# Optimization experiments

Measured on AMD Instinct MI355X. Metric: run time of the kernel, lower is better.

## Reference

```python
import jax, jax.numpy as jnp
import numpy as np

N_NODES = 50000
N_EDGES = 800000
D_IN = 64
D_OUT = 64


def setup_inputs() -> dict:
    key = jax.random.key(0)
    k = jax.random.split(key, 5)
    stdv = 1.0 / np.sqrt(D_OUT)
    X = jax.random.normal(k[0], (N_NODES, D_IN), jnp.float32)
    weights = jax.random.uniform(k[1], (D_IN, D_OUT), jnp.float32, -stdv, stdv)
    attention_w = jax.random.normal(k[2], (1, 1), jnp.float32)
    # edge list: row = destination (segment) ids, sorted (CSR-like); col = source ids
    row = jnp.sort(jax.random.randint(k[3], (N_EDGES,), 0, N_NODES, jnp.int32))
    col = jax.random.randint(k[4], (N_EDGES,), 0, N_NODES, jnp.int32)
    return {"X": X, "weights": weights, "attention_w": attention_w, "row": row, "col": col}


def reference(X, weights, attention_w, row, col):
    # dense linear
    Xp = X @ weights  # [N, D_OUT]
    # SDDMM: per-edge dot product between dst and src transformed features
    edge_feature = jnp.einsum('ed,ed->e', Xp[row], Xp[col])  # [E]
    # scale by scalar attention weight (n_heads = 1)
    edge_attn = edge_feature * attention_w[0, 0]  # [E]
    # SpMM aggregation: out[i] = sum_{e: row[e]=i} edge_attn[e] * Xp[col[e]]
    out = jax.ops.segment_sum(edge_attn[:, None] * Xp[col], row,
                              num_segments=X.shape[0])  # [N, D_OUT]
    return out
```

## Files before the change

### kernel.cpp

```cpp
#include <hip/hip_runtime.h>
#include <hip/hip_fp16.h>

#define D 64

typedef _Float16 h16;
typedef h16 h16x2 __attribute__((ext_vector_type(2)));

__device__ __forceinline__ h16x2 u2h(unsigned int u) {
    union { unsigned int i; h16x2 h; } t; t.i = u; return t.h;
}

__device__ __forceinline__ float dot8_f16(uint4 a, uint4 b, float c) {
#if __has_builtin(__builtin_amdgcn_fdot2)
    c = __builtin_amdgcn_fdot2(u2h(a.x), u2h(b.x), c, false);
    c = __builtin_amdgcn_fdot2(u2h(a.y), u2h(b.y), c, false);
    c = __builtin_amdgcn_fdot2(u2h(a.z), u2h(b.z), c, false);
    c = __builtin_amdgcn_fdot2(u2h(a.w), u2h(b.w), c, false);
    return c;
#else
    float2 t;
    t = __half22float2(*(const __half2*)&a.x); float2 s = __half22float2(*(const __half2*)&b.x);
    c = fmaf(t.x, s.x, c); c = fmaf(t.y, s.y, c);
    t = __half22float2(*(const __half2*)&a.y); s = __half22float2(*(const __half2*)&b.y);
    c = fmaf(t.x, s.x, c); c = fmaf(t.y, s.y, c);
    t = __half22float2(*(const __half2*)&a.z); s = __half22float2(*(const __half2*)&b.z);
    c = fmaf(t.x, s.x, c); c = fmaf(t.y, s.y, c);
    t = __half22float2(*(const __half2*)&a.w); s = __half22float2(*(const __half2*)&b.w);
    c = fmaf(t.x, s.x, c); c = fmaf(t.y, s.y, c);
    return c;
#endif
}

__device__ __forceinline__ void h8_to_f32(uint4 u, float f[8]) {
    float2 t;
    t = __half22float2(*(const __half2*)&u.x); f[0] = t.x; f[1] = t.y;
    t = __half22float2(*(const __half2*)&u.y); f[2] = t.x; f[3] = t.y;
    t = __half22float2(*(const __half2*)&u.z); f[4] = t.x; f[5] = t.y;
    t = __half22float2(*(const __half2*)&u.w); f[6] = t.x; f[7] = t.y;
}

__global__ __launch_bounds__(256) void prep_kernel(const float* __restrict__ X,
                                                   const float* __restrict__ W,
                                                   const int* __restrict__ row,
                                                   __half* __restrict__ Xp,
                                                   int* __restrict__ rowptr,
                                                   int nNodes, int nEdges,
                                                   int gemmBlocks) {
    if ((int)blockIdx.x >= gemmBlocks) {
        int e = (blockIdx.x - gemmBlocks) * 256 + threadIdx.x;
        if (e >= nEdges) return;
        int r = row[e];
        int rprev = (e == 0) ? -1 : row[e - 1];
        for (int q = rprev + 1; q <= r; ++q) rowptr[q] = e;
        if (e == nEdges - 1) {
            for (int q = r + 1; q <= nNodes; ++q) rowptr[q] = nEdges;
        }
        return;
    }
    int lane = threadIdx.x & 63;
    int wave = (blockIdx.x * 256 + threadIdx.x) >> 6;
    int nWaves = gemmBlocks * 4;

    float w[D];
#pragma unroll
    for (int k = 0; k < D; ++k) w[k] = W[k * D + lane];

    for (int r = wave; r < nNodes; r += nWaves) {
        int rr = __builtin_amdgcn_readfirstlane(r);
        const float4* xr = (const float4*)(X + (size_t)rr * D);
        float acc = 0.f;
#pragma unroll
        for (int k4 = 0; k4 < D / 4; ++k4) {
            float4 xv = xr[k4];
            acc = fmaf(xv.x, w[4 * k4 + 0], acc);
            acc = fmaf(xv.y, w[4 * k4 + 1], acc);
            acc = fmaf(xv.z, w[4 * k4 + 2], acc);
            acc = fmaf(xv.w, w[4 * k4 + 3], acc);
        }
        Xp[(size_t)rr * D + lane] = __float2half(acc);
    }
}

__global__ __launch_bounds__(256) void fused_kernel(const __half* __restrict__ Xp,
                                                    const int* __restrict__ rowptr,
                                                    const int* __restrict__ col,
                                                    const float* __restrict__ attn_w,
                                                    float* __restrict__ out,
                                                    int nNodes) {
    int lane = threadIdx.x & 63;
    int waveId = (blockIdx.x * 256 + threadIdx.x) >> 6;
    int g = lane >> 3;
    int j = lane & 7;

    int node = waveId * 8 + g;
    bool active = node < nNodes;
    int nd = active ? node : 0;

    int eStart = rowptr[nd];
    int eEnd   = active ? rowptr[nd + 1] : eStart;

    const uint4* XpV = (const uint4*)Xp;
    uint4 xr = XpV[(size_t)nd * 8 + j];

    float acc[8] = {0.f, 0.f, 0.f, 0.f, 0.f, 0.f, 0.f, 0.f};

    bool v[4]; uint4 raw[4];
#pragma unroll
    for (int u = 0; u < 4; ++u) {
        int ee = eStart + u;
        v[u] = ee < eEnd;
        int cc = col[v[u] ? ee : 0];
        raw[u] = XpV[(size_t)cc * 8 + j];
    }

    for (int e = eStart; e < eEnd; e += 4) {
        bool v2[4]; uint4 raw2[4];
#pragma unroll
        for (int u = 0; u < 4; ++u) {
            int ee = e + 4 + u;
            v2[u] = ee < eEnd;
            int cc = col[v2[u] ? ee : 0];
            raw2[u] = XpV[(size_t)cc * 8 + j];
        }
        float p[4];
#pragma unroll
        for (int u = 0; u < 4; ++u) p[u] = dot8_f16(xr, raw[u], 0.f);
#pragma unroll
        for (int off = 1; off < 8; off <<= 1)
#pragma unroll
            for (int u = 0; u < 4; ++u) p[u] += __shfl_xor(p[u], off, 64);
#pragma unroll
        for (int u = 0; u < 4; ++u) {
            float s = v[u] ? p[u] : 0.f;
            float xf[8]; h8_to_f32(raw[u], xf);
#pragma unroll
            for (int q = 0; q < 8; ++q) acc[q] = fmaf(s, xf[q], acc[q]);
        }
#pragma unroll
        for (int u = 0; u < 4; ++u) { v[u] = v2[u]; raw[u] = raw2[u]; }
    }

    if (active) {
        float attn = attn_w[0];
        float4* o = (float4*)(out + (size_t)node * D + 8 * j);
        o[0] = make_float4(attn * acc[0], attn * acc[1], attn * acc[2], attn * acc[3]);
        o[1] = make_float4(attn * acc[4], attn * acc[5], attn * acc[6], attn * acc[7]);
    }
}

extern "C" void kernel_launch(void* const* d_in, const int* in_sizes, int n_in,
                              void* d_out, int out_size, void* d_ws, size_t ws_size,
                              hipStream_t stream) {
    const float* X    = (const float*)d_in[0];
    const float* W    = (const float*)d_in[1];
    const float* attn = (const float*)d_in[2];
    const int*   row  = (const int*)d_in[3];
    const int*   col  = (const int*)d_in[4];
    float* out = (float*)d_out;

    int nNodes = in_sizes[0] / D;
    int nEdges = in_sizes[3];

    __half* Xp  = (__half*)d_ws;
    int* rowptr = (int*)((char*)d_ws + (size_t)nNodes * D * sizeof(__half));

    int gemmBlocks = 1024;
    int rpBlocks   = (nEdges + 255) / 256;
    prep_kernel<<<gemmBlocks + rpBlocks, 256, 0, stream>>>(X, W, row, Xp, rowptr,
                                                           nNodes, nEdges, gemmBlocks);

    int waves = (nNodes + 7) / 8;
    fused_kernel<<<(waves + 3) / 4, 256, 0, stream>>>(Xp, rowptr, col, attn, out, nNodes);
}
```

Measured before the change: 104.0 us.

## Split each node's edge range across two lane groups and reduce via shuffle

```diff
diff --git a/kernel.cpp b/kernel.cpp
--- a/kernel.cpp
+++ b/kernel.cpp
@@ -5,6 +5,7 @@
 
 typedef _Float16 h16;
 typedef h16 h16x2 __attribute__((ext_vector_type(2)));
+typedef float f32x4 __attribute__((ext_vector_type(4)));
 
 __device__ __forceinline__ h16x2 u2h(unsigned int u) {
     union { unsigned int i; h16x2 h; } t; t.i = u; return t.h;
@@ -31,12 +32,10 @@
 #endif
 }
 
-__device__ __forceinline__ void h8_to_f32(uint4 u, float f[8]) {
-    float2 t;
-    t = __half22float2(*(const __half2*)&u.x); f[0] = t.x; f[1] = t.y;
-    t = __half22float2(*(const __half2*)&u.y); f[2] = t.x; f[3] = t.y;
-    t = __half22float2(*(const __half2*)&u.z); f[4] = t.x; f[5] = t.y;
-    t = __half22float2(*(const __half2*)&u.w); f[6] = t.x; f[7] = t.y;
+__device__ __forceinline__ void fma8_mix(uint4 x, float s, float acc[8]) {
+    union { uint4 u; __half h[8]; } t; t.u = x;
+#pragma unroll
+    for (int q = 0; q < 8; ++q) acc[q] = fmaf(__half2float(t.h[q]), s, acc[q]);
 }
 
 __global__ __launch_bounds__(256) void prep_kernel(const float* __restrict__ X,
@@ -91,13 +90,18 @@
     int waveId = (blockIdx.x * 256 + threadIdx.x) >> 6;
     int g = lane >> 3;
     int j = lane & 7;
+    int slot = g >> 1;
+    int half = g & 1;
 
-    int node = waveId * 8 + g;
+    int node = waveId * 4 + slot;
     bool active = node < nNodes;
     int nd = active ? node : 0;
 
-    int eStart = rowptr[nd];
-    int eEnd   = active ? rowptr[nd + 1] : eStart;
+    int s0 = rowptr[nd];
+    int e0 = active ? rowptr[nd + 1] : s0;
+    int mid = s0 + ((e0 - s0 + 1) >> 1);
+    int eStart = half ? mid : s0;
+    int eEnd   = half ? e0  : mid;
 
     const uint4* XpV = (const uint4*)Xp;
     uint4 xr = XpV[(size_t)nd * 8 + j];
@@ -132,19 +136,22 @@
 #pragma unroll
         for (int u = 0; u < 4; ++u) {
             float s = v[u] ? p[u] : 0.f;
-            float xf[8]; h8_to_f32(raw[u], xf);
-#pragma unroll
-            for (int q = 0; q < 8; ++q) acc[q] = fmaf(s, xf[q], acc[q]);
+            fma8_mix(raw[u], s, acc);
         }
 #pragma unroll
         for (int u = 0; u < 4; ++u) { v[u] = v2[u]; raw[u] = raw2[u]; }
     }
 
-    if (active) {
+#pragma unroll
+    for (int q = 0; q < 8; ++q) acc[q] += __shfl_xor(acc[q], 8, 64);
+
+    if (active && half == 0) {
         float attn = attn_w[0];
-        float4* o = (float4*)(out + (size_t)node * D + 8 * j);
-        o[0] = make_float4(attn * acc[0], attn * acc[1], attn * acc[2], attn * acc[3]);
-        o[1] = make_float4(attn * acc[4], attn * acc[5], attn * acc[6], attn * acc[7]);
+        f32x4* o = (f32x4*)(out + (size_t)node * D + 8 * j);
+        f32x4 o0 = {attn * acc[0], attn * acc[1], attn * acc[2], attn * acc[3]};
+        f32x4 o1 = {attn * acc[4], attn * acc[5], attn * acc[6], attn * acc[7]};
+        __builtin_nontemporal_store(o0, o);
+        __builtin_nontemporal_store(o1, o + 1);
     }
 }
 
@@ -169,6 +176,6 @@
     prep_kernel<<<gemmBlocks + rpBlocks, 256, 0, stream>>>(X, W, row, Xp, rowptr,
                                                            nNodes, nEdges, gemmBlocks);
 
-    int waves = (nNodes + 7) / 8;
+    int waves = (nNodes + 3) / 4;
     fused_kernel<<<(waves + 3) / 4, 256, 0, stream>>>(Xp, rowptr, col, attn, out, nNodes);
 }
```

Result: no change. 103.4 us (-0.6%).
